# Optimization experiments

Measured on AMD Instinct MI355X. Metric: run time of the kernel, lower is better.

## Reference

```python
import jax, jax.numpy as jnp
import numpy as np

N_NODES = 100000
N_EDGES = 3200000
IN_F, HID_F, OUT_F = 512, 64, 16


def setup_inputs() -> dict:
    key = jax.random.key(0)
    k1, k2, k3, k4 = jax.random.split(key, 4)
    x = jax.random.normal(k1, (N_NODES, IN_F), dtype=jnp.float32)
    edge_index = jax.random.randint(k2, (2, N_EDGES), 0, N_NODES, dtype=jnp.int64)
    W1 = jax.random.normal(k3, (IN_F, HID_F), dtype=jnp.float32) * (1.0 / np.sqrt(IN_F))
    b1 = jnp.zeros((HID_F,), dtype=jnp.float32)
    W2 = jax.random.normal(k4, (HID_F, OUT_F), dtype=jnp.float32) * (1.0 / np.sqrt(HID_F))
    b2 = jnp.zeros((OUT_F,), dtype=jnp.float32)
    return {"x": x, "edge_index": edge_index, "W1": W1, "b1": b1, "W2": W2, "b2": b2}


def _gcn_norm(edge_index, n_nodes):
    # add self-loops (GCNConv default), edge_weight = 1
    loop = jnp.arange(n_nodes, dtype=edge_index.dtype)
    src = jnp.concatenate([edge_index[0], loop])
    dst = jnp.concatenate([edge_index[1], loop])
    ones = jnp.ones(src.shape[0], dtype=jnp.float32)
    deg = jax.ops.segment_sum(ones, dst, num_segments=n_nodes)
    dinv = jnp.where(deg > 0, jax.lax.rsqrt(deg), 0.0)
    norm = dinv[src] * dinv[dst]  # symmetric normalization D^-1/2 A D^-1/2
    return src, dst, norm


def _gcn_conv(h, src, dst, norm, W, b, n_nodes):
    h = h @ W                                 # project first (small GEMM)
    msg = h[src] * norm[:, None]              # gather + scale  [E+N, F_out]
    agg = jax.ops.segment_sum(msg, dst, num_segments=n_nodes)  # scatter-add
    return agg + b


def reference(x, edge_index, W1, b1, W2, b2):
    n = x.shape[0]
    src, dst, norm = _gcn_norm(edge_index, n)
    h = jax.nn.relu(_gcn_conv(x, src, dst, norm, W1, b1, n))
    # F.dropout with training=False is identity (eval-mode reference)
    h = _gcn_conv(h, src, dst, norm, W2, b2, n)
    return jax.nn.log_softmax(h, axis=1)
```

## Files before the change

kernel.cpp:

```cpp
#include <hip/hip_runtime.h>

#define NN   100000
#define NE   3200000
#define INF_ 512
#define HIDF 64
#define OUTF 16
#define BR    128
#define NBUCK ((NN + BR - 1) / BR)
#define BSLOT 4864
#define NSLOT 72
#define EBLK  16384
#define NFB   ((NE + EBLK - 1) / EBLK)

typedef __bf16 bf16x8 __attribute__((ext_vector_type(8)));
typedef float  f32x4  __attribute__((ext_vector_type(4)));

__device__ inline unsigned short f2bfu(float f) {
    unsigned u = __builtin_bit_cast(unsigned, f);
    u += 0x7FFFu + ((u >> 16) & 1u);
    return (unsigned short)(u >> 16);
}
__device__ inline __bf16 bfbits(unsigned short h) {
    return __builtin_bit_cast(__bf16, h);
}
__device__ inline float bf2f(unsigned short h) {
    unsigned u = (unsigned)h << 16;
    return __builtin_bit_cast(float, u);
}

__global__ __launch_bounds__(256) void k_binit(int* __restrict__ bcur) {
    int b = blockIdx.x * 256 + threadIdx.x;
    if (b < NBUCK) bcur[b] = b * BSLOT;
}

__global__ __launch_bounds__(256) void k_wconv(const float* __restrict__ W1,
                                               unsigned short* __restrict__ w1c) {
    int i = blockIdx.x * 256 + threadIdx.x;
    if (i < INF_ * HIDF) {
        int k = i >> 6, n = i & 63;
        w1c[((k >> 2) * 64 + n) * 4 + (k & 3)] = f2bfu(W1[i]);
    }
}

__global__ __launch_bounds__(256) void k_fillA(const int* __restrict__ src,
                                               const int* __restrict__ dst,
                                               int* __restrict__ bcur,
                                               unsigned int* __restrict__ pairs) {
    __shared__ int hist[NBUCK];
    __shared__ int rbase[NBUCK];
    int t = threadIdx.x;
    int e0 = blockIdx.x * EBLK;
    int e1 = (e0 + EBLK < NE) ? e0 + EBLK : NE;

    for (int b = t; b < NBUCK; b += 256) hist[b] = 0;
    __syncthreads();
    for (int e = e0 + t; e < e1; e += 256)
        atomicAdd(&hist[dst[e] >> 7], 1);
    __syncthreads();
    for (int b = t; b < NBUCK; b += 256) {
        int c = hist[b];
        rbase[b] = c ? atomicAdd(&bcur[b], c) : 0;
        hist[b] = 0;
    }
    __syncthreads();
    for (int e = e0 + t; e < e1; e += 256) {
        int s = src[e], d = dst[e];
        int b = d >> 7;
        int slot = atomicAdd(&hist[b], 1);
        pairs[rbase[b] + slot] = ((unsigned)s << 7) | (unsigned)(d & 127);
    }
}

__global__ __launch_bounds__(256) void k_fillB(const int* __restrict__ bcur,
                                               const unsigned int* __restrict__ pairs,
                                               int* __restrict__ re,
                                               float* __restrict__ dinv,
                                               int* __restrict__ csr) {
    __shared__ int cur_s[BR];
    int b  = blockIdx.x;
    int t  = threadIdx.x;
    int n0 = b * BR;
    int ncount = ((n0 + BR < NN) ? BR : NN - n0);
    int gbase = b * BSLOT;
    int gend  = bcur[b];

    if (t < BR) cur_s[t] = (n0 + t) * NSLOT;
    __syncthreads();

    for (int j = gbase + t; j < gend; j += 256) {
        unsigned int p = pairs[j];
        int pos = atomicAdd(&cur_s[p & 127u], 1);
        csr[pos] = (int)(p >> 7);
    }
    __syncthreads();

    if (t < ncount) {
        int endp = cur_s[t];
        int n = n0 + t;
        re[n]   = endp;
        dinv[n] = rsqrtf((float)(endp - n * NSLOT + 1));
    }
}

#define GM 64

__global__ __launch_bounds__(256) void k_gemm1(const float* __restrict__ x,
                                               const unsigned short* __restrict__ w1c,
                                               const float* __restrict__ dinv,
                                               unsigned short* __restrict__ h1s) {
    __shared__ unsigned short bs[8192];
    int t    = threadIdx.x;
    int lane = t & 63;
    int w    = t >> 6;
    int m    = lane & 15;
    int kg   = lane >> 4;
    int mb   = blockIdx.x * GM;

    int rowi = mb + w * 16 + m;
    size_t xrow = (size_t)((rowi < NN) ? rowi : NN - 1);
    const float* xp = x + xrow * INF_ + kg * 4;

    f32x4 acc0 = {0.f,0.f,0.f,0.f}, acc1 = acc0, acc2 = acc0, acc3 = acc0;

    const uint4* w1c4 = (const uint4*)w1c;
    uint4* bs4 = (uint4*)bs;

    for (int kc = 0; kc < 4; ++kc) {
#pragma unroll
        for (int i = 0; i < 4; ++i)
            bs4[t + i * 256] = w1c4[kc * 1024 + t + i * 256];
        __syncthreads();

#pragma unroll
        for (int ks = 0; ks < 4; ++ks) {
            int ksg = kc * 4 + ks;
            float4 xa = *(const float4*)(xp + ksg * 32);
            float4 xb = *(const float4*)(xp + ksg * 32 + 16);
            bf16x8 A;
            A[0] = bfbits(f2bfu(xa.x)); A[1] = bfbits(f2bfu(xa.y));
            A[2] = bfbits(f2bfu(xa.z)); A[3] = bfbits(f2bfu(xa.w));
            A[4] = bfbits(f2bfu(xb.x)); A[5] = bfbits(f2bfu(xb.y));
            A[6] = bfbits(f2bfu(xb.z)); A[7] = bfbits(f2bfu(xb.w));

            int qq0 = ks * 8 + kg;
            int qq1 = qq0 + 4;
#pragma unroll
            for (int n0t = 0; n0t < 4; ++n0t) {
                ushort4 b0 = *(const ushort4*)&bs[(qq0 * 64 + n0t * 16 + m) * 4];
                ushort4 b1 = *(const ushort4*)&bs[(qq1 * 64 + n0t * 16 + m) * 4];
                bf16x8 B;
                B[0] = bfbits(b0.x); B[1] = bfbits(b0.y);
                B[2] = bfbits(b0.z); B[3] = bfbits(b0.w);
                B[4] = bfbits(b1.x); B[5] = bfbits(b1.y);
                B[6] = bfbits(b1.z); B[7] = bfbits(b1.w);
                f32x4 c = (n0t == 0) ? acc0 : (n0t == 1) ? acc1 : (n0t == 2) ? acc2 : acc3;
                c = __builtin_amdgcn_mfma_f32_16x16x32_bf16(A, B, c, 0, 0, 0);
                if      (n0t == 0) acc0 = c;
                else if (n0t == 1) acc1 = c;
                else if (n0t == 2) acc2 = c;
                else               acc3 = c;
            }
        }
        __syncthreads();
    }

#pragma unroll
    for (int r = 0; r < 4; ++r) {
        int node = mb + w * 16 + kg * 4 + r;
        if (node < NN) {
            float dv = dinv[node];
            size_t o = (size_t)node * HIDF + m;
            h1s[o +  0] = f2bfu(acc0[r] * dv);
            h1s[o + 16] = f2bfu(acc1[r] * dv);
            h1s[o + 32] = f2bfu(acc2[r] * dv);
            h1s[o + 48] = f2bfu(acc3[r] * dv);
        }
    }
}

__global__ __launch_bounds__(256) void k_hid2(const int* __restrict__ re,
                                              const int* __restrict__ csr,
                                              const float* __restrict__ dinv,
                                              const unsigned short* __restrict__ h1s,
                                              const float* __restrict__ b1,
                                              const float* __restrict__ W2,
                                              unsigned short* __restrict__ h2s) {
    __shared__ float w2s[HIDF * OUTF];
    __shared__ float b1s[HIDF];
    __shared__ float hbuf[4][HIDF];
    int t = threadIdx.x;
    for (int i = t; i < HIDF * OUTF; i += 256) w2s[i] = W2[i];
    if (t < HIDF) b1s[t] = b1[t];
    __syncthreads();

    int l = t & 63;
    int w = t >> 6;
    int g = l >> 4;
    int q = l & 15;
    int n = __builtin_amdgcn_readfirstlane(blockIdx.x * 4 + w);
    int row = n * NSLOT;
    int end = re[n];
    float dn = dinv[n];

    float a0 = 0.f, a1 = 0.f, a2 = 0.f, a3 = 0.f;

    int j = row;
    for (; j + 8 <= end; j += 8) {
        int4 scA = *(const int4*)&csr[j];
        int4 scB = *(const int4*)&csr[j + 4];
        int sA = (g & 2) ? ((g & 1) ? scA.w : scA.z) : ((g & 1) ? scA.y : scA.x);
        int sB = (g & 2) ? ((g & 1) ? scB.w : scB.z) : ((g & 1) ? scB.y : scB.x);
        ushort4 hA = *(const ushort4*)&h1s[(unsigned)(sA * HIDF + q * 4)];
        ushort4 hB = *(const ushort4*)&h1s[(unsigned)(sB * HIDF + q * 4)];
        a0 += bf2f(hA.x) + bf2f(hB.x);
        a1 += bf2f(hA.y) + bf2f(hB.y);
        a2 += bf2f(hA.z) + bf2f(hB.z);
        a3 += bf2f(hA.w) + bf2f(hB.w);
    }
    if (j + 4 <= end) {
        int4 sc = *(const int4*)&csr[j];
        int s = (g & 2) ? ((g & 1) ? sc.w : sc.z) : ((g & 1) ? sc.y : sc.x);
        ushort4 h = *(const ushort4*)&h1s[(unsigned)(s * HIDF + q * 4)];
        a0 += bf2f(h.x); a1 += bf2f(h.y); a2 += bf2f(h.z); a3 += bf2f(h.w);
        j += 4;
    }
    if (j + g < end) {
        int s = csr[j + g];
        ushort4 h = *(const ushort4*)&h1s[(unsigned)(s * HIDF + q * 4)];
        a0 += bf2f(h.x); a1 += bf2f(h.y); a2 += bf2f(h.z); a3 += bf2f(h.w);
    }

    a0 += __shfl_xor(a0, 16); a1 += __shfl_xor(a1, 16);
    a2 += __shfl_xor(a2, 16); a3 += __shfl_xor(a3, 16);
    a0 += __shfl_xor(a0, 32); a1 += __shfl_xor(a1, 32);
    a2 += __shfl_xor(a2, 32); a3 += __shfl_xor(a3, 32);

    ushort4 hs = *(const ushort4*)&h1s[(unsigned)(n * HIDF + q * 4)];
    a0 = fmaxf(fmaf(dn, a0 + bf2f(hs.x), b1s[q * 4 + 0]), 0.f);
    a1 = fmaxf(fmaf(dn, a1 + bf2f(hs.y), b1s[q * 4 + 1]), 0.f);
    a2 = fmaxf(fmaf(dn, a2 + bf2f(hs.z), b1s[q * 4 + 2]), 0.f);
    a3 = fmaxf(fmaf(dn, a3 + bf2f(hs.w), b1s[q * 4 + 3]), 0.f);
    if (g == 0) *(float4*)&hbuf[w][q * 4] = make_float4(a0, a1, a2, a3);
    __syncthreads();

    int o  = l & 15;
    int kg = l >> 4;
    const float* hb = hbuf[w];
    float s = 0.f;
#pragma unroll
    for (int i = 0; i < 16; ++i) {
        int k = kg * 16 + i;
        s = fmaf(hb[k], w2s[k * OUTF + o], s);
    }
    s += __shfl_xor(s, 16);
    s += __shfl_xor(s, 32);
    if (l < 16) h2s[(unsigned)(n * OUTF + o)] = f2bfu(dn * s);
}

__global__ __launch_bounds__(256) void k_out2(const int* __restrict__ re,
                                              const int* __restrict__ csr,
                                              const float* __restrict__ dinv,
                                              const unsigned short* __restrict__ h2s,
                                              const float* __restrict__ b2,
                                              float* __restrict__ out) {
    int t = blockIdx.x * 256 + threadIdx.x;
    int n = t >> 4;
    int f = t & 15;
    if (n >= NN) return;
    int row = n * NSLOT, end = re[n];
    float dn = dinv[n];
    float acc = bf2f(h2s[(unsigned)(n * OUTF + f)]);

    int j = row;
    for (; j + 4 <= end; j += 4) {
        int s0 = csr[j], s1 = csr[j + 1], s2 = csr[j + 2], s3 = csr[j + 3];
        float v0 = bf2f(h2s[(unsigned)(s0 * OUTF + f)]);
        float v1 = bf2f(h2s[(unsigned)(s1 * OUTF + f)]);
        float v2 = bf2f(h2s[(unsigned)(s2 * OUTF + f)]);
        float v3 = bf2f(h2s[(unsigned)(s3 * OUTF + f)]);
        acc += (v0 + v1) + (v2 + v3);
    }
    for (; j < end; ++j)
        acc += bf2f(h2s[(unsigned)(csr[j] * OUTF + f)]);

    float v = fmaf(dn, acc, b2[f]);

    float m = v;
#pragma unroll
    for (int mask = 1; mask < 16; mask <<= 1)
        m = fmaxf(m, __shfl_xor(m, mask, 16));
    float ex = __expf(v - m);
    float s  = ex;
#pragma unroll
    for (int mask = 1; mask < 16; mask <<= 1)
        s += __shfl_xor(s, mask, 16);
    out[(size_t)n * OUTF + f] = v - (m + __logf(s));
}

extern "C" void kernel_launch(void* const* d_in, const int* in_sizes, int n_in,
                              void* d_out, int out_size, void* d_ws, size_t ws_size,
                              hipStream_t stream) {
    const float* x  = (const float*)d_in[0];
    const int*   ei = (const int*)d_in[1];
    const float* W1 = (const float*)d_in[2];
    const float* b1 = (const float*)d_in[3];
    const float* W2 = (const float*)d_in[4];
    const float* b2 = (const float*)d_in[5];
    float*       out = (float*)d_out;

    char*  ws = (char*)d_ws;
    size_t o  = 0;
    auto alloc = [&](size_t bytes) {
        void* p = ws + o;
        o = (o + bytes + 1023) & ~(size_t)1023;
        return p;
    };
    int*            bcur  = (int*)           alloc((size_t)NBUCK * 4);
    int*            re    = (int*)           alloc((size_t)NN * 4);
    int*            csr   = (int*)           alloc((size_t)NN * NSLOT * 4);
    unsigned int*   pairs = (unsigned int*)  alloc((size_t)NBUCK * BSLOT * 4);
    float*          dinv  = (float*)         alloc((size_t)NN * 4);
    unsigned short* w1c   = (unsigned short*)alloc((size_t)INF_ * HIDF * 2);
    unsigned short* h1s   = (unsigned short*)alloc((size_t)NN * HIDF * 2);
    unsigned short* h2s   = (unsigned short*)alloc((size_t)NN * OUTF * 2);
    if (o > ws_size) return;

    const int* esrc = ei;
    const int* edst = ei + NE;

    k_binit <<<(NBUCK + 255) / 256, 256, 0, stream>>>(bcur);
    k_wconv <<<(INF_ * HIDF + 255) / 256, 256, 0, stream>>>(W1, w1c);
    k_fillA <<<NFB, 256, 0, stream>>>(esrc, edst, bcur, pairs);
    k_fillB <<<NBUCK, 256, 0, stream>>>(bcur, pairs, re, dinv, csr);

    k_gemm1 <<<(NN + GM - 1) / GM, 256, 0, stream>>>(x, w1c, dinv, h1s);
    k_hid2  <<<NN / 4, 256, 0, stream>>>(re, csr, dinv, h1s, b1, W2, h2s);
    k_out2  <<<(NN * OUTF + 255) / 256, 256, 0, stream>>>(re, csr, dinv, h2s, b2, out);
}
```

Baseline: 267.1 us.

## Stage x tiles through double-buffered swizzled LDS with register prefetch in gemm1

```diff
diff --git a/kernel.cpp b/kernel.cpp
--- a/kernel.cpp
+++ b/kernel.cpp
@@ -109,6 +109,7 @@
                                                const float* __restrict__ dinv,
                                                unsigned short* __restrict__ h1s) {
     __shared__ unsigned short bs[8192];
+    __shared__ float xs[2][2048];
     int t    = threadIdx.x;
     int lane = t & 63;
     int w    = t >> 6;
@@ -116,52 +117,83 @@
     int kg   = lane >> 4;
     int mb   = blockIdx.x * GM;
 
-    int rowi = mb + w * 16 + m;
-    size_t xrow = (size_t)((rowi < NN) ? rowi : NN - 1);
-    const float* xp = x + xrow * INF_ + kg * 4;
+    int sr = t >> 3;
+    int sg = t & 7;
+    int rowg0 = mb + sr;        if (rowg0 >= NN) rowg0 = NN - 1;
+    int rowg1 = mb + sr + 32;   if (rowg1 >= NN) rowg1 = NN - 1;
+    const float* gx0 = x + (size_t)rowg0 * INF_ + sg * 4;
+    const float* gx1 = x + (size_t)rowg1 * INF_ + sg * 4;
+    int ls0 = sr * 32 + ((sg ^ (sr & 7)) << 2);
+    int ls1 = (sr + 32) * 32 + ((sg ^ ((sr + 32) & 7)) << 2);
+
+    int rowA = w * 16 + m;
+    int sw1 = ((kg ^ (m & 7)) << 2);
+    int sw2 = (((kg + 4) ^ (m & 7)) << 2);
+    const float* xr = &xs[0][0];
 
     f32x4 acc0 = {0.f,0.f,0.f,0.f}, acc1 = acc0, acc2 = acc0, acc3 = acc0;
 
     const uint4* w1c4 = (const uint4*)w1c;
     uint4* bs4 = (uint4*)bs;
 
-    for (int kc = 0; kc < 4; ++kc) {
-#pragma unroll
-        for (int i = 0; i < 4; ++i)
-            bs4[t + i * 256] = w1c4[kc * 1024 + t + i * 256];
+    {
+        float4 p0 = *(const float4*)(gx0);
+        float4 p1 = *(const float4*)(gx1);
+        *(float4*)&xs[0][ls0] = p0;
+        *(float4*)&xs[0][ls1] = p1;
+    }
+
+    int buf = 0;
+    for (int sk = 0; sk < 16; ++sk) {
+        int kc  = sk >> 2;
+        int ksl = sk & 3;
+        if (ksl == 0) {
+            if (sk) __syncthreads();
+#pragma unroll
+            for (int i = 0; i < 4; ++i)
+                bs4[t + i * 256] = w1c4[kc * 1024 + t + i * 256];
+        }
         __syncthreads();
 
-#pragma unroll
-        for (int ks = 0; ks < 4; ++ks) {
-            int ksg = kc * 4 + ks;
-            float4 xa = *(const float4*)(xp + ksg * 32);
-            float4 xb = *(const float4*)(xp + ksg * 32 + 16);
-            bf16x8 A;
-            A[0] = bfbits(f2bfu(xa.x)); A[1] = bfbits(f2bfu(xa.y));
-            A[2] = bfbits(f2bfu(xa.z)); A[3] = bfbits(f2bfu(xa.w));
-            A[4] = bfbits(f2bfu(xb.x)); A[5] = bfbits(f2bfu(xb.y));
-            A[6] = bfbits(f2bfu(xb.z)); A[7] = bfbits(f2bfu(xb.w));
-
-            int qq0 = ks * 8 + kg;
-            int qq1 = qq0 + 4;
-#pragma unroll
-            for (int n0t = 0; n0t < 4; ++n0t) {
-                ushort4 b0 = *(const ushort4*)&bs[(qq0 * 64 + n0t * 16 + m) * 4];
-                ushort4 b1 = *(const ushort4*)&bs[(qq1 * 64 + n0t * 16 + m) * 4];
-                bf16x8 B;
-                B[0] = bfbits(b0.x); B[1] = bfbits(b0.y);
-                B[2] = bfbits(b0.z); B[3] = bfbits(b0.w);
-                B[4] = bfbits(b1.x); B[5] = bfbits(b1.y);
-                B[6] = bfbits(b1.z); B[7] = bfbits(b1.w);
-                f32x4 c = (n0t == 0) ? acc0 : (n0t == 1) ? acc1 : (n0t == 2) ? acc2 : acc3;
-                c = __builtin_amdgcn_mfma_f32_16x16x32_bf16(A, B, c, 0, 0, 0);
-                if      (n0t == 0) acc0 = c;
-                else if (n0t == 1) acc1 = c;
-                else if (n0t == 2) acc2 = c;
-                else               acc3 = c;
-            }
-        }
-        __syncthreads();
+        float4 p0, p1;
+        if (sk < 15) {
+            p0 = *(const float4*)(gx0 + (sk + 1) * 32);
+            p1 = *(const float4*)(gx1 + (sk + 1) * 32);
+        }
+
+        const float* xb_ = &xs[buf][0];
+        float4 xa = *(const float4*)&xb_[rowA * 32 + sw1];
+        float4 xbv = *(const float4*)&xb_[rowA * 32 + sw2];
+        bf16x8 A;
+        A[0] = bfbits(f2bfu(xa.x));  A[1] = bfbits(f2bfu(xa.y));
+        A[2] = bfbits(f2bfu(xa.z));  A[3] = bfbits(f2bfu(xa.w));
+        A[4] = bfbits(f2bfu(xbv.x)); A[5] = bfbits(f2bfu(xbv.y));
+        A[6] = bfbits(f2bfu(xbv.z)); A[7] = bfbits(f2bfu(xbv.w));
+
+        int qq0 = ksl * 8 + kg;
+        int qq1 = qq0 + 4;
+#pragma unroll
+        for (int n0t = 0; n0t < 4; ++n0t) {
+            ushort4 b0 = *(const ushort4*)&bs[(qq0 * 64 + n0t * 16 + m) * 4];
+            ushort4 b1 = *(const ushort4*)&bs[(qq1 * 64 + n0t * 16 + m) * 4];
+            bf16x8 B;
+            B[0] = bfbits(b0.x); B[1] = bfbits(b0.y);
+            B[2] = bfbits(b0.z); B[3] = bfbits(b0.w);
+            B[4] = bfbits(b1.x); B[5] = bfbits(b1.y);
+            B[6] = bfbits(b1.z); B[7] = bfbits(b1.w);
+            f32x4 c = (n0t == 0) ? acc0 : (n0t == 1) ? acc1 : (n0t == 2) ? acc2 : acc3;
+            c = __builtin_amdgcn_mfma_f32_16x16x32_bf16(A, B, c, 0, 0, 0);
+            if      (n0t == 0) acc0 = c;
+            else if (n0t == 1) acc1 = c;
+            else if (n0t == 2) acc2 = c;
+            else               acc3 = c;
+        }
+
+        if (sk < 15) {
+            *(float4*)&xs[buf ^ 1][ls0] = p0;
+            *(float4*)&xs[buf ^ 1][ls1] = p1;
+        }
+        buf ^= 1;
     }
 
 #pragma unroll
@@ -176,6 +208,7 @@
             h1s[o + 48] = f2bfu(acc3[r] * dv);
         }
     }
+    (void)xr;
 }
 
 __global__ __launch_bounds__(256) void k_hid2(const int* __restrict__ re,
```

New measurement: 270.4 us. About the same (+1.2%).

## Split bucket cursors into per-group slices and deepen gather unrolling

Applied to the files above, without the earlier changes.

```diff
diff --git a/kernel.cpp b/kernel.cpp
--- a/kernel.cpp
+++ b/kernel.cpp
@@ -1,13 +1,16 @@
 #include <hip/hip_runtime.h>
 
-#define NN   100000
-#define NE   3200000
-#define INF_ 512
-#define HIDF 64
-#define OUTF 16
+#define NN    100000
+#define NE    3200000
+#define INF_  512
+#define HIDF  64
+#define OUTF  16
 #define BR    128
 #define NBUCK ((NN + BR - 1) / BR)
-#define BSLOT 4864
+#define NGRP  8
+#define SLICE 704
+#define BSLOT (NGRP * SLICE)
+#define NCUR  (NBUCK * NGRP)
 #define NSLOT 72
 #define EBLK  16384
 #define NFB   ((NE + EBLK - 1) / EBLK)
@@ -29,8 +32,8 @@
 }
 
 __global__ __launch_bounds__(256) void k_binit(int* __restrict__ bcur) {
-    int b = blockIdx.x * 256 + threadIdx.x;
-    if (b < NBUCK) bcur[b] = b * BSLOT;
+    int i = blockIdx.x * 256 + threadIdx.x;
+    if (i < NCUR) bcur[i] = (i >> 3) * BSLOT + (i & 7) * SLICE;
 }
 
 __global__ __launch_bounds__(256) void k_wconv(const float* __restrict__ W1,
@@ -51,6 +54,7 @@
     int t = threadIdx.x;
     int e0 = blockIdx.x * EBLK;
     int e1 = (e0 + EBLK < NE) ? e0 + EBLK : NE;
+    int grp = (int)(((long long)blockIdx.x * NGRP) / NFB);
 
     for (int b = t; b < NBUCK; b += 256) hist[b] = 0;
     __syncthreads();
@@ -59,7 +63,7 @@
     __syncthreads();
     for (int b = t; b < NBUCK; b += 256) {
         int c = hist[b];
-        rbase[b] = c ? atomicAdd(&bcur[b], c) : 0;
+        rbase[b] = c ? atomicAdd(&bcur[b * NGRP + grp], c) : 0;
         hist[b] = 0;
     }
     __syncthreads();
@@ -81,16 +85,18 @@
     int t  = threadIdx.x;
     int n0 = b * BR;
     int ncount = ((n0 + BR < NN) ? BR : NN - n0);
-    int gbase = b * BSLOT;
-    int gend  = bcur[b];
 
     if (t < BR) cur_s[t] = (n0 + t) * NSLOT;
     __syncthreads();
 
-    for (int j = gbase + t; j < gend; j += 256) {
-        unsigned int p = pairs[j];
-        int pos = atomicAdd(&cur_s[p & 127u], 1);
-        csr[pos] = (int)(p >> 7);
+    for (int g = 0; g < NGRP; ++g) {
+        int s0 = b * BSLOT + g * SLICE;
+        int s1 = bcur[b * NGRP + g];
+        for (int j = s0 + t; j < s1; j += 256) {
+            unsigned int p = pairs[j];
+            int pos = atomicAdd(&cur_s[p & 127u], 1);
+            csr[pos] = (int)(p >> 7);
+        }
     }
     __syncthreads();
 
@@ -205,6 +211,24 @@
     float a0 = 0.f, a1 = 0.f, a2 = 0.f, a3 = 0.f;
 
     int j = row;
+    for (; j + 16 <= end; j += 16) {
+        int4 scA = *(const int4*)&csr[j];
+        int4 scB = *(const int4*)&csr[j + 4];
+        int4 scC = *(const int4*)&csr[j + 8];
+        int4 scD = *(const int4*)&csr[j + 12];
+        int sA = (g & 2) ? ((g & 1) ? scA.w : scA.z) : ((g & 1) ? scA.y : scA.x);
+        int sB = (g & 2) ? ((g & 1) ? scB.w : scB.z) : ((g & 1) ? scB.y : scB.x);
+        int sC = (g & 2) ? ((g & 1) ? scC.w : scC.z) : ((g & 1) ? scC.y : scC.x);
+        int sD = (g & 2) ? ((g & 1) ? scD.w : scD.z) : ((g & 1) ? scD.y : scD.x);
+        ushort4 hA = *(const ushort4*)&h1s[(unsigned)(sA * HIDF + q * 4)];
+        ushort4 hB = *(const ushort4*)&h1s[(unsigned)(sB * HIDF + q * 4)];
+        ushort4 hC = *(const ushort4*)&h1s[(unsigned)(sC * HIDF + q * 4)];
+        ushort4 hD = *(const ushort4*)&h1s[(unsigned)(sD * HIDF + q * 4)];
+        a0 += (bf2f(hA.x) + bf2f(hB.x)) + (bf2f(hC.x) + bf2f(hD.x));
+        a1 += (bf2f(hA.y) + bf2f(hB.y)) + (bf2f(hC.y) + bf2f(hD.y));
+        a2 += (bf2f(hA.z) + bf2f(hB.z)) + (bf2f(hC.z) + bf2f(hD.z));
+        a3 += (bf2f(hA.w) + bf2f(hB.w)) + (bf2f(hC.w) + bf2f(hD.w));
+    }
     for (; j + 8 <= end; j += 8) {
         int4 scA = *(const int4*)&csr[j];
         int4 scB = *(const int4*)&csr[j + 4];
@@ -272,6 +296,19 @@
     float acc = bf2f(h2s[(unsigned)(n * OUTF + f)]);
 
     int j = row;
+    for (; j + 8 <= end; j += 8) {
+        int s0 = csr[j],     s1 = csr[j + 1], s2 = csr[j + 2], s3 = csr[j + 3];
+        int s4 = csr[j + 4], s5 = csr[j + 5], s6 = csr[j + 6], s7 = csr[j + 7];
+        float v0 = bf2f(h2s[(unsigned)(s0 * OUTF + f)]);
+        float v1 = bf2f(h2s[(unsigned)(s1 * OUTF + f)]);
+        float v2 = bf2f(h2s[(unsigned)(s2 * OUTF + f)]);
+        float v3 = bf2f(h2s[(unsigned)(s3 * OUTF + f)]);
+        float v4 = bf2f(h2s[(unsigned)(s4 * OUTF + f)]);
+        float v5 = bf2f(h2s[(unsigned)(s5 * OUTF + f)]);
+        float v6 = bf2f(h2s[(unsigned)(s6 * OUTF + f)]);
+        float v7 = bf2f(h2s[(unsigned)(s7 * OUTF + f)]);
+        acc += ((v0 + v1) + (v2 + v3)) + ((v4 + v5) + (v6 + v7));
+    }
     for (; j + 4 <= end; j += 4) {
         int s0 = csr[j], s1 = csr[j + 1], s2 = csr[j + 2], s3 = csr[j + 3];
         float v0 = bf2f(h2s[(unsigned)(s0 * OUTF + f)]);
@@ -315,7 +352,7 @@
         o = (o + bytes + 1023) & ~(size_t)1023;
         return p;
     };
-    int*            bcur  = (int*)           alloc((size_t)NBUCK * 4);
+    int*            bcur  = (int*)           alloc((size_t)NCUR * 4);
     int*            re    = (int*)           alloc((size_t)NN * 4);
     int*            csr   = (int*)           alloc((size_t)NN * NSLOT * 4);
     unsigned int*   pairs = (unsigned int*)  alloc((size_t)NBUCK * BSLOT * 4);
@@ -328,7 +365,7 @@
     const int* esrc = ei;
     const int* edst = ei + NE;
 
-    k_binit <<<(NBUCK + 255) / 256, 256, 0, stream>>>(bcur);
+    k_binit <<<(NCUR + 255) / 256, 256, 0, stream>>>(bcur);
     k_wconv <<<(INF_ * HIDF + 255) / 256, 256, 0, stream>>>(W1, w1c);
     k_fillA <<<NFB, 256, 0, stream>>>(esrc, edst, bcur, pairs);
     k_fillB <<<NBUCK, 256, 0, stream>>>(bcur, pairs, re, dinv, csr);
```

Result: faster. 259.6 us (-2.8%).
